# Kernel tuning notes

Hardware: AMD Instinct MI355X
Metric: run time of the kernel (lower is better)

Reference implementation:

```python
import jax, jax.numpy as jnp
import numpy as np

H = 16  # num attention heads
D = 1024  # hidden size
F = 4096  # intermediate size
LN_EPS = 1e-5


def _glorot(key, shape):
    fan_in, fan_out = shape[0], shape[1]
    lim = np.sqrt(6.0 / (fan_in + fan_out))
    return jax.random.uniform(key, shape, jnp.float32, -lim, lim)


def setup_inputs() -> dict:
    key = jax.random.key(0)
    ks = jax.random.split(key, 16)
    inp = {
        'input_tensor': jax.random.normal(ks[0], (4, 1024, D), jnp.float32),
        'ctx_tensor': jax.random.normal(ks[1], (4, 2048, D), jnp.float32),
        'ctx_attn_mask': jnp.zeros((4, 1, 1, 2048), jnp.float32),
        # cross-attention QKV
        'cq_w': _glorot(ks[2], (D, D)), 'cq_b': jnp.zeros((D,)),
        'ck_w': _glorot(ks[3], (D, D)), 'ck_b': jnp.zeros((D,)),
        'cv_w': _glorot(ks[4], (D, D)), 'cv_b': jnp.zeros((D,)),
        # cross output (dense + LN)
        'co_w': _glorot(ks[5], (D, D)), 'co_b': jnp.zeros((D,)),
        'co_g': jnp.ones((D,)), 'co_be': jnp.zeros((D,)),
        # self-attention QKV
        'sq_w': _glorot(ks[6], (D, D)), 'sq_b': jnp.zeros((D,)),
        'sk_w': _glorot(ks[7], (D, D)), 'sk_b': jnp.zeros((D,)),
        'sv_w': _glorot(ks[8], (D, D)), 'sv_b': jnp.zeros((D,)),
        # self-attention output
        'so_w': _glorot(ks[9], (D, D)), 'so_b': jnp.zeros((D,)),
        'so_g': jnp.ones((D,)), 'so_be': jnp.zeros((D,)),
        # FFN intermediate + output
        'fi_w': _glorot(ks[10], (D, F)), 'fi_b': jnp.zeros((F,)),
        'fo_w': _glorot(ks[11], (F, D)), 'fo_b': jnp.zeros((D,)),
        'fo_g': jnp.ones((D,)), 'fo_be': jnp.zeros((D,)),
    }
    return inp


def _split_heads(x):
    b, l, _ = x.shape
    return x.reshape(b, l, H, D // H)


def _mha(x, ctx, mask, qw, qb, kw, kb, vw, vb):
    # manual QK^T/sqrt(d) -> +mask -> softmax -> V (dropout=0 / eval)
    q = _split_heads(x @ qw + qb)       # [b, lq, h, d]
    k = _split_heads(ctx @ kw + kb)     # [b, lk, h, d]
    v = _split_heads(ctx @ vw + vb)
    scores = jnp.einsum('bqhd,bkhd->bhqk', q, k) / np.sqrt(D // H).astype(np.float32)
    if mask is not None:
        scores = scores + mask
    probs = jax.nn.softmax(scores, axis=-1)
    out = jnp.einsum('bhqk,bkhd->bqhd', probs, v)
    return out.reshape(x.shape[0], x.shape[1], D)


def _self_output(h, residual, w, b, g, be):
    h = h @ w + b
    h = h + residual
    mu = jnp.mean(h, axis=-1, keepdims=True)
    var = jnp.mean(jnp.square(h - mu), axis=-1, keepdims=True)
    return (h - mu) * jax.lax.rsqrt(var + LN_EPS) * g + be


def reference(input_tensor, ctx_tensor, ctx_attn_mask,
              cq_w, cq_b, ck_w, ck_b, cv_w, cv_b, co_w, co_b, co_g, co_be,
              sq_w, sq_b, sk_w, sk_b, sv_w, sv_b, so_w, so_b, so_g, so_be,
              fi_w, fi_b, fo_w, fo_b, fo_g, fo_be):
    # CrossLayer.forward
    ca = _mha(input_tensor, ctx_tensor, ctx_attn_mask, cq_w, cq_b, ck_w, ck_b, cv_w, cv_b)
    x = _self_output(ca, input_tensor, co_w, co_b, co_g, co_be)
    sa = _mha(x, x, None, sq_w, sq_b, sk_w, sk_b, sv_w, sv_b)
    x = _self_output(sa, x, so_w, so_b, so_g, so_be)
    inter = jax.nn.gelu(x @ fi_w + fi_b, approximate=False)
    x = _self_output(inter, x, fo_w, fo_b, fo_g, fo_be)
    return x
```

## Files before the change

kernel.cpp:

```cpp
#include <hip/hip_runtime.h>
#include <math.h>

typedef unsigned short ushort_t;
typedef __bf16 bf16x8 __attribute__((ext_vector_type(8)));
typedef float f32x4 __attribute__((ext_vector_type(4)));

__device__ __forceinline__ float bf2f(unsigned int u) {
    union { unsigned int i; float f; } v; v.i = u << 16; return v.f;
}
__device__ __forceinline__ ushort_t f2bf(float f) {
    union { float f; unsigned int i; } v; v.f = f;
    unsigned int u = v.i;
    unsigned int r = u + 0x7fffu + ((u >> 16) & 1u);
    return (ushort_t)(r >> 16);
}
__device__ __forceinline__ ushort_t f2bf_hw(float f) {
    union { __bf16 h; ushort_t u; } v; v.h = (__bf16)f; return v.u;
}

template <int N>
__device__ __forceinline__ float ror16f(float x) {
    union { float f; int i; } u; u.f = x;
    u.i = __builtin_amdgcn_mov_dpp(u.i, 0x120 + N, 0xF, 0xF, true);
    return u.f;
}

__device__ __forceinline__ void gload16(const ushort_t* g, ushort_t* l) {
    __builtin_amdgcn_global_load_lds(
        (__attribute__((address_space(1))) void*)g,
        (__attribute__((address_space(3))) void*)l, 16, 0, 0);
}

__global__ void __launch_bounds__(256) cvt_bf16_kernel(
    const float* __restrict__ in, ushort_t* __restrict__ out, int n8)
{
    int i = blockIdx.x * 256 + threadIdx.x;
    if (i >= n8) return;
    size_t off = (size_t)i * 8;
    float4 a = *(const float4*)(in + off);
    float4 b = *(const float4*)(in + off + 4);
    ushort_t o[8] = {f2bf(a.x), f2bf(a.y), f2bf(a.z), f2bf(a.w),
                     f2bf(b.x), f2bf(b.y), f2bf(b.z), f2bf(b.w)};
    *(uint4*)(out + off) = *(const uint4*)o;
}

__global__ void __launch_bounds__(256) wconv_kernel(
    const float* __restrict__ W, ushort_t* __restrict__ Wt, int K, int N)
{
    __shared__ float tile[32][33];
    const int t = threadIdx.x;
    const int k0 = blockIdx.x * 32, n0 = blockIdx.y * 32;
    const int r = t >> 3, c4 = (t & 7) * 4;
    float4 d = *(const float4*)(&W[(size_t)(k0 + r) * N + n0 + c4]);
    tile[r][c4 + 0] = d.x; tile[r][c4 + 1] = d.y;
    tile[r][c4 + 2] = d.z; tile[r][c4 + 3] = d.w;
    __syncthreads();
    ushort_t o[4] = { f2bf(tile[c4 + 0][r]), f2bf(tile[c4 + 1][r]),
                      f2bf(tile[c4 + 2][r]), f2bf(tile[c4 + 3][r]) };
    *(uint2*)(&Wt[(size_t)(n0 + r) * K + k0 + c4]) = *(const uint2*)o;
}

template <int MODE, int BMT, int BNT, int BKT>
__global__ void __launch_bounds__(256) gemm_bt_kernel(
    const ushort_t* __restrict__ A,
    const ushort_t* __restrict__ B0, const ushort_t* __restrict__ B1,
    const ushort_t* __restrict__ B2,
    const float* __restrict__ bias0, const float* __restrict__ bias1,
    const float* __restrict__ bias2,
    ushort_t* __restrict__ C0, ushort_t* __restrict__ C1,
    ushort_t* __restrict__ C2,
    int M, int N, int K)
{
    __shared__ __align__(16) ushort_t As[2][BMT * BKT];
    __shared__ __align__(16) ushort_t Bs[2][BNT * BKT];

    constexpr int WM = BMT / 2;
    constexpr int MIF = WM / 16;
    constexpr int WN = BNT / 2;
    constexpr int NJF = WN / 16;
    constexpr int KK = BKT / 32;
    constexpr int CPR = BKT / 8;
    constexpr int PA = BMT * BKT / 2048;
    constexpr int PB = BNT * BKT / 2048;
    constexpr int LPT = PA + PB;

    const int z = blockIdx.z;
    const ushort_t* Bt = (z == 0) ? B0 : ((z == 1) ? B1 : B2);
    const float* bias = (z == 0) ? bias0 : ((z == 1) ? bias1 : bias2);
    ushort_t* Cout = (z == 0) ? C0 : ((z == 1) ? C1 : C2);

    const int tid = threadIdx.x;
    const int m0 = blockIdx.y * BMT, n0 = blockIdx.x * BNT;
    const int wave = tid >> 6, lane = tid & 63;
    const int wm = wave >> 1, wn = wave & 1;
    const int lr = lane & 15;
    const int lk = (lane >> 4) * 8;

    const ushort_t* Ab = A + (size_t)m0 * K;
    const ushort_t* Bb = Bt + (size_t)n0 * K;

    f32x4 acc[MIF][NJF];
#pragma unroll
    for (int i = 0; i < MIF; i++)
#pragma unroll
        for (int j = 0; j < NJF; j++) acc[i][j] = (f32x4){0.f, 0.f, 0.f, 0.f};

    const int nt = K / BKT;

    auto stage = [&](int buf, int t) {
#pragma unroll
        for (int p = 0; p < PA; p++) {
            int v = p * 256 + tid;
            int row = v / CPR, c = v % CPR;
            gload16(Ab + (size_t)row * K + (size_t)t * BKT + c * 8,
                    &As[buf][v * 8]);
        }
#pragma unroll
        for (int p = 0; p < PB; p++) {
            int v = p * 256 + tid;
            int row = v / CPR, c = v % CPR;
            gload16(Bb + (size_t)row * K + (size_t)t * BKT + c * 8,
                    &Bs[buf][v * 8]);
        }
    };

    stage(0, 0);

    for (int t = 0; t < nt; ++t) {
        const int p = t & 1;
        if (t + 1 < nt) {
            stage(p ^ 1, t + 1);
            asm volatile("s_waitcnt vmcnt(%0)" :: "n"(LPT) : "memory");
        } else {
            asm volatile("s_waitcnt vmcnt(0)" ::: "memory");
        }
        __builtin_amdgcn_s_barrier();

        bf16x8 af[MIF][KK], bfr[NJF][KK];
#pragma unroll
        for (int i = 0; i < MIF; i++)
#pragma unroll
            for (int kk = 0; kk < KK; kk++)
                af[i][kk] = *(const bf16x8*)(&As[p][(wm * WM + i * 16 + lr) * BKT + kk * 32 + lk]);
#pragma unroll
        for (int j = 0; j < NJF; j++)
#pragma unroll
            for (int kk = 0; kk < KK; kk++)
                bfr[j][kk] = *(const bf16x8*)(&Bs[p][(wn * WN + j * 16 + lr) * BKT + kk * 32 + lk]);
#pragma unroll
        for (int kk = 0; kk < KK; kk++)
#pragma unroll
            for (int i = 0; i < MIF; i++)
#pragma unroll
                for (int j = 0; j < NJF; j++)
                    acc[i][j] = __builtin_amdgcn_mfma_f32_16x16x32_bf16(af[i][kk], bfr[j][kk], acc[i][j], 0, 0, 0);

        asm volatile("" ::: "memory");
        __builtin_amdgcn_s_barrier();
    }

    const int rq = (lane >> 4) * 4;
#pragma unroll
    for (int j = 0; j < NJF; j++) {
        const int col = n0 + wn * WN + j * 16 + lr;
        const float bv = bias[col];
#pragma unroll
        for (int i = 0; i < MIF; i++) {
#pragma unroll
            for (int r = 0; r < 4; r++) {
                const int row = m0 + wm * WM + i * 16 + rq + r;
                float v = acc[i][j][r] + bv;
                if (MODE == 2) {
                    v = 0.5f * v * (1.0f + erff(v * 0.70710678118654752f));
                }
                Cout[(size_t)row * N + col] = f2bf(v);
            }
        }
    }
}

__global__ void __launch_bounds__(256) mfma_attn_kernel(
    const ushort_t* __restrict__ Q, const ushort_t* __restrict__ Kt,
    const ushort_t* __restrict__ Vt, const float* __restrict__ mask,
    ushort_t* __restrict__ O, int Lq, int Lk, float scale)
{
    __shared__ __align__(16) ushort_t qs[64][72];
    __shared__ __align__(16) ushort_t ks[64][72];
    __shared__ __align__(16) ushort_t vsT[64][72];
    __shared__ __align__(16) ushort_t ps[4][16][72];

    const int tid = threadIdx.x;
    const int wave = tid >> 6, lane = tid & 63;
    const int quad = lane >> 4, lc = lane & 15;

    const int id = blockIdx.x + (int)gridDim.x * blockIdx.y;
    const int bh = (id & 7) * 8 + ((id >> 3) >> 4);
    const int qt = (id >> 3) & 15;
    const int b = bh >> 4, h = bh & 15;
    const int q0 = qt * 64;
    const size_t qbase = ((size_t)b * Lq) * 1024 + h * 64;
    const size_t kbase = ((size_t)b * Lk) * 1024 + h * 64;
    const float* maskb = mask ? (mask + (size_t)b * Lk) : nullptr;

#pragma unroll
    for (int r = 0; r < 2; r++) {
        int v = r * 256 + tid;
        int row = v >> 3, c8 = (v & 7) * 8;
        *(uint4*)(&qs[row][c8]) = *(const uint4*)(&Q[qbase + (size_t)(q0 + row) * 1024 + c8]);
    }
    __syncthreads();

    bf16x8 qa0 = *(const bf16x8*)(&qs[wave * 16 + lc][quad * 8]);
    bf16x8 qa1 = *(const bf16x8*)(&qs[wave * 16 + lc][32 + quad * 8]);

    f32x4 o[4];
#pragma unroll
    for (int d = 0; d < 4; d++) o[d] = (f32x4){0.f, 0.f, 0.f, 0.f};
    float m_i[4], l_i[4];
#pragma unroll
    for (int r = 0; r < 4; r++) { m_i[r] = -1e30f; l_i[r] = 0.f; }

    const int sr = tid >> 2;
    const int d0c = (tid & 3) * 16;
    const int vswz = (tid & 3) << 3;
    const int vcol = sr ^ vswz;

    const int nt = Lk >> 6;
    size_t gk = kbase + (size_t)sr * 1024 + d0c;

    uint4 kA = *(const uint4*)(Kt + gk);
    uint4 kB = *(const uint4*)(Kt + gk + 8);
    uint4 vA = *(const uint4*)(Vt + gk);
    uint4 vB = *(const uint4*)(Vt + gk + 8);

    for (int t = 0; t < nt; ++t) {
        const int kt = t << 6;
        __syncthreads();
        *(uint4*)(&ks[sr][d0c])     = kA;
        *(uint4*)(&ks[sr][d0c + 8]) = kB;
        {
            const ushort_t* vp = (const ushort_t*)&vA;
            const ushort_t* wp = (const ushort_t*)&vB;
#pragma unroll
            for (int i = 0; i < 8; i++) vsT[d0c + i][vcol]     = vp[i];
#pragma unroll
            for (int i = 0; i < 8; i++) vsT[d0c + 8 + i][vcol] = wp[i];
        }
        if (t + 1 < nt) {
            gk += 64 * 1024;
            kA = *(const uint4*)(Kt + gk);
            kB = *(const uint4*)(Kt + gk + 8);
            vA = *(const uint4*)(Vt + gk);
            vB = *(const uint4*)(Vt + gk + 8);
        }
        __syncthreads();

        float mk[4];
#pragma unroll
        for (int g = 0; g < 4; g++)
            mk[g] = maskb ? maskb[kt + g * 16 + lc] : 0.f;

        f32x4 s[4];
        __builtin_amdgcn_s_setprio(1);
#pragma unroll
        for (int g = 0; g < 4; g++) {
            bf16x8 k0 = *(const bf16x8*)(&ks[g * 16 + lc][quad * 8]);
            bf16x8 k1 = *(const bf16x8*)(&ks[g * 16 + lc][32 + quad * 8]);
            f32x4 zz = (f32x4){0.f, 0.f, 0.f, 0.f};
            zz = __builtin_amdgcn_mfma_f32_16x16x32_bf16(qa0, k0, zz, 0, 0, 0);
            zz = __builtin_amdgcn_mfma_f32_16x16x32_bf16(qa1, k1, zz, 0, 0, 0);
            s[g] = zz;
        }
        __builtin_amdgcn_s_setprio(0);

        float alpha[4];
#pragma unroll
        for (int r = 0; r < 4; r++) {
            float v0 = s[0][r] * scale + mk[0];
            float v1 = s[1][r] * scale + mk[1];
            float v2 = s[2][r] * scale + mk[2];
            float v3 = s[3][r] * scale + mk[3];
            float mx = fmaxf(fmaxf(v0, v1), fmaxf(v2, v3));
            mx = fmaxf(mx, ror16f<1>(mx));
            mx = fmaxf(mx, ror16f<2>(mx));
            mx = fmaxf(mx, ror16f<4>(mx));
            mx = fmaxf(mx, ror16f<8>(mx));
            float mnew = fmaxf(m_i[r], mx);
            alpha[r] = __expf(m_i[r] - mnew);
            m_i[r] = mnew;
            float p0 = __expf(v0 - mnew);
            float p1 = __expf(v1 - mnew);
            float p2 = __expf(v2 - mnew);
            float p3 = __expf(v3 - mnew);
            ps[wave][quad * 4 + r][lc]      = f2bf_hw(p0);
            ps[wave][quad * 4 + r][16 + lc] = f2bf_hw(p1);
            ps[wave][quad * 4 + r][32 + lc] = f2bf_hw(p2);
            ps[wave][quad * 4 + r][48 + lc] = f2bf_hw(p3);
            float psum = (p0 + p1) + (p2 + p3);
            psum += ror16f<1>(psum);
            psum += ror16f<2>(psum);
            psum += ror16f<4>(psum);
            psum += ror16f<8>(psum);
            l_i[r] = l_i[r] * alpha[r] + psum;
        }
#pragma unroll
        for (int d = 0; d < 4; d++)
#pragma unroll
            for (int r = 0; r < 4; r++) o[d][r] *= alpha[r];

        __builtin_amdgcn_s_setprio(1);
#pragma unroll
        for (int kk = 0; kk < 2; kk++) {
            bf16x8 pa = *(const bf16x8*)(&ps[wave][lc][kk * 32 + quad * 8]);
#pragma unroll
            for (int d = 0; d < 4; d++) {
                int dr = d * 16 + lc;
                bf16x8 vb = *(const bf16x8*)(&vsT[dr][(kk * 32 + quad * 8) ^ (d << 3)]);
                o[d] = __builtin_amdgcn_mfma_f32_16x16x32_bf16(pa, vb, o[d], 0, 0, 0);
            }
        }
        __builtin_amdgcn_s_setprio(0);
    }

#pragma unroll
    for (int d = 0; d < 4; d++) {
#pragma unroll
        for (int r = 0; r < 4; r++) {
            float val = o[d][r] / l_i[r];
            O[qbase + (size_t)(q0 + wave * 16 + quad * 4 + r) * 1024 + d * 16 + lc] = f2bf_hw(val);
        }
    }
}

template <bool RES_F32, bool OUT_F32>
__global__ void __launch_bounds__(256) ln_kernel(
    const ushort_t* __restrict__ Hbuf, const void* __restrict__ Res,
    const float* __restrict__ gamma, const float* __restrict__ beta,
    void* __restrict__ Out)
{
    const int row = blockIdx.x;
    const int tid = threadIdx.x;
    const size_t base = (size_t)row * 1024 + tid * 4;

    uint2 hh = *(const uint2*)(Hbuf + base);
    float v[4];
    v[0] = bf2f(hh.x & 0xffffu);
    v[1] = bf2f(hh.x >> 16);
    v[2] = bf2f(hh.y & 0xffffu);
    v[3] = bf2f(hh.y >> 16);
    if (RES_F32) {
        float4 rv = *(const float4*)((const float*)Res + base);
        v[0] += rv.x; v[1] += rv.y; v[2] += rv.z; v[3] += rv.w;
    } else {
        uint2 rr = *(const uint2*)((const ushort_t*)Res + base);
        v[0] += bf2f(rr.x & 0xffffu);
        v[1] += bf2f(rr.x >> 16);
        v[2] += bf2f(rr.y & 0xffffu);
        v[3] += bf2f(rr.y >> 16);
    }

    float s = v[0] + v[1] + v[2] + v[3];
    float s2 = v[0]*v[0] + v[1]*v[1] + v[2]*v[2] + v[3]*v[3];
#pragma unroll
    for (int o = 1; o < 64; o <<= 1) {
        s += __shfl_xor(s, o, 64);
        s2 += __shfl_xor(s2, o, 64);
    }
    __shared__ float red[8];
    const int wv = tid >> 6, ln_ = tid & 63;
    if (ln_ == 0) { red[wv] = s; red[wv + 4] = s2; }
    __syncthreads();
    s = red[0] + red[1] + red[2] + red[3];
    s2 = red[4] + red[5] + red[6] + red[7];
    const float mu = s * (1.0f / 1024.0f);
    const float var = s2 * (1.0f / 1024.0f) - mu * mu;
    const float rstd = rsqrtf(var + 1e-5f);

    float4 gv = *(const float4*)(&gamma[tid * 4]);
    float4 bv = *(const float4*)(&beta[tid * 4]);
    float o0 = (v[0] - mu) * rstd * gv.x + bv.x;
    float o1 = (v[1] - mu) * rstd * gv.y + bv.y;
    float o2 = (v[2] - mu) * rstd * gv.z + bv.z;
    float o3 = (v[3] - mu) * rstd * gv.w + bv.w;

    if (OUT_F32) {
        float4 of = {o0, o1, o2, o3};
        *(float4*)((float*)Out + base) = of;
    } else {
        ushort_t ob[4] = {f2bf(o0), f2bf(o1), f2bf(o2), f2bf(o3)};
        *(uint2*)((ushort_t*)Out + base) = *(uint2*)ob;
    }
}

extern "C" void kernel_launch(void* const* d_in, const int* in_sizes, int n_in,
                              void* d_out, int out_size, void* d_ws, size_t ws_size,
                              hipStream_t stream)
{
    const float* input = (const float*)d_in[0];
    const float* ctx   = (const float*)d_in[1];
    const float* mask  = (const float*)d_in[2];
    const float* cq_w = (const float*)d_in[3],  *cq_b = (const float*)d_in[4];
    const float* ck_w = (const float*)d_in[5],  *ck_b = (const float*)d_in[6];
    const float* cv_w = (const float*)d_in[7],  *cv_b = (const float*)d_in[8];
    const float* co_w = (const float*)d_in[9],  *co_b = (const float*)d_in[10];
    const float* co_g = (const float*)d_in[11], *co_be = (const float*)d_in[12];
    const float* sq_w = (const float*)d_in[13], *sq_b = (const float*)d_in[14];
    const float* sk_w = (const float*)d_in[15], *sk_b = (const float*)d_in[16];
    const float* sv_w = (const float*)d_in[17], *sv_b = (const float*)d_in[18];
    const float* so_w = (const float*)d_in[19], *so_b = (const float*)d_in[20];
    const float* so_g = (const float*)d_in[21], *so_be = (const float*)d_in[22];
    const float* fi_w = (const float*)d_in[23], *fi_b = (const float*)d_in[24];
    const float* fo_w = (const float*)d_in[25], *fo_b = (const float*)d_in[26];
    const float* fo_g = (const float*)d_in[27], *fo_be = (const float*)d_in[28];

    char* p = (char*)d_ws;
    const size_t MB = 1024 * 1024;
    ushort_t* Bq   = (ushort_t*)(p + 0 * MB);
    ushort_t* Bk   = (ushort_t*)(p + 8 * MB);
    ushort_t* Bv   = (ushort_t*)(p + 24 * MB);
    ushort_t* Ba   = (ushort_t*)(p + 40 * MB);
    ushort_t* Bh   = (ushort_t*)(p + 48 * MB);
    ushort_t* Bx1  = (ushort_t*)(p + 56 * MB);
    ushort_t* Bx2  = (ushort_t*)(p + 64 * MB);
    ushort_t* Bi   = Bk;
    ushort_t* Xctx = Ba;
    ushort_t* Xin  = Bx2;
    ushort_t* WtA  = (ushort_t*)(p + 56 * MB);
    ushort_t* WtB  = (ushort_t*)(p + 58 * MB);
    ushort_t* WtC  = (ushort_t*)(p + 60 * MB);
    ushort_t* WtD  = (ushort_t*)(p + 64 * MB);
    ushort_t* WtE  = (ushort_t*)(p + 66 * MB);
    ushort_t* WtF  = (ushort_t*)(p + 68 * MB);
    ushort_t* WtG  = (ushort_t*)(p + 0 * MB);

    const float scale = 0.125f;
    dim3 blk(256);

    cvt_bf16_kernel<<<2048, blk, 0, stream>>>(input, Xin, 524288);
    cvt_bf16_kernel<<<4096, blk, 0, stream>>>(ctx, Xctx, 1048576);

    wconv_kernel<<<dim3(32, 32), blk, 0, stream>>>(cq_w, WtA, 1024, 1024);
    wconv_kernel<<<dim3(32, 32), blk, 0, stream>>>(ck_w, WtB, 1024, 1024);
    wconv_kernel<<<dim3(32, 32), blk, 0, stream>>>(cv_w, WtC, 1024, 1024);
    gemm_bt_kernel<0, 64, 64, 64><<<dim3(16, 64, 1), blk, 0, stream>>>(
        Xin, WtA, WtA, WtA, cq_b, cq_b, cq_b, Bq, Bq, Bq, 4096, 1024, 1024);
    gemm_bt_kernel<0, 64, 64, 64><<<dim3(16, 128, 2), blk, 0, stream>>>(
        Xctx, WtB, WtC, WtC, ck_b, cv_b, cv_b, Bk, Bv, Bv, 8192, 1024, 1024);
    mfma_attn_kernel<<<dim3(16, 64), blk, 0, stream>>>(Bq, Bk, Bv, mask, Ba, 1024, 2048, scale);
    wconv_kernel<<<dim3(32, 32), blk, 0, stream>>>(co_w, WtA, 1024, 1024);
    gemm_bt_kernel<0, 64, 64, 64><<<dim3(16, 64, 1), blk, 0, stream>>>(
        Ba, WtA, WtA, WtA, co_b, co_b, co_b, Bh, Bh, Bh, 4096, 1024, 1024);
    ln_kernel<true, false><<<dim3(4096), blk, 0, stream>>>(Bh, input, co_g, co_be, Bx1);

    wconv_kernel<<<dim3(32, 32), blk, 0, stream>>>(sq_w, WtD, 1024, 1024);
    wconv_kernel<<<dim3(32, 32), blk, 0, stream>>>(sk_w, WtE, 1024, 1024);
    wconv_kernel<<<dim3(32, 32), blk, 0, stream>>>(sv_w, WtF, 1024, 1024);
    gemm_bt_kernel<0, 64, 64, 64><<<dim3(16, 64, 3), blk, 0, stream>>>(
        Bx1, WtD, WtE, WtF, sq_b, sk_b, sv_b, Bq, Bk, Bv, 4096, 1024, 1024);
    mfma_attn_kernel<<<dim3(16, 64), blk, 0, stream>>>(Bq, Bk, Bv, nullptr, Ba, 1024, 1024, scale);
    wconv_kernel<<<dim3(32, 32), blk, 0, stream>>>(so_w, WtD, 1024, 1024);
    gemm_bt_kernel<0, 64, 64, 64><<<dim3(16, 64, 1), blk, 0, stream>>>(
        Ba, WtD, WtD, WtD, so_b, so_b, so_b, Bh, Bh, Bh, 4096, 1024, 1024);
    ln_kernel<false, false><<<dim3(4096), blk, 0, stream>>>(Bh, Bx1, so_g, so_be, Bx2);

    wconv_kernel<<<dim3(32, 128), blk, 0, stream>>>(fi_w, WtG, 1024, 4096);
    gemm_bt_kernel<2, 128, 128, 32><<<dim3(32, 32, 1), blk, 0, stream>>>(
        Bx2, WtG, WtG, WtG, fi_b, fi_b, fi_b, Bi, Bi, Bi, 4096, 4096, 1024);
    wconv_kernel<<<dim3(128, 32), blk, 0, stream>>>(fo_w, WtG, 4096, 1024);
    gemm_bt_kernel<0, 64, 64, 64><<<dim3(16, 64, 1), blk, 0, stream>>>(
        Bi, WtG, WtG, WtG, fo_b, fo_b, fo_b, Bh, Bh, Bh, 4096, 1024, 4096);
    ln_kernel<false, true><<<dim3(4096), blk, 0, stream>>>(Bh, Bx2, fo_g, fo_be, (float*)d_out);
}
```

Baseline: 699.3 us.

## Merge cross-attention QKV GEMMs, enlarge GEMM M-tile, add lazy softmax rescale

The GEMM kernel now takes two A inputs with per-z row counts, so the cross-attention Q projection (4096 rows) and the K/V projections (8192 rows) run as one launch, with blocks past a slice's rows exiting early. The 1024-wide GEMMs move from 64x64 to 128x64 tiles to get more reuse per block. In flash attention, the running max and the rescale of the output accumulator are skipped when the new block max exceeds the old one by no more than 8 across the wave. This removes exp and multiply work, at the cost of fewer GEMM blocks for occupancy and a looser bound on exponent growth.

```diff
diff --git a/kernel.cpp b/kernel.cpp
--- a/kernel.cpp
+++ b/kernel.cpp
@@ -62,14 +62,15 @@
 
 template <int MODE, int BMT, int BNT, int BKT>
 __global__ void __launch_bounds__(256) gemm_bt_kernel(
-    const ushort_t* __restrict__ A,
+    const ushort_t* __restrict__ A0, const ushort_t* __restrict__ A1,
+    int M0, int M1,
     const ushort_t* __restrict__ B0, const ushort_t* __restrict__ B1,
     const ushort_t* __restrict__ B2,
     const float* __restrict__ bias0, const float* __restrict__ bias1,
     const float* __restrict__ bias2,
     ushort_t* __restrict__ C0, ushort_t* __restrict__ C1,
     ushort_t* __restrict__ C2,
-    int M, int N, int K)
+    int N, int K)
 {
     __shared__ __align__(16) ushort_t As[2][BMT * BKT];
     __shared__ __align__(16) ushort_t Bs[2][BNT * BKT];
@@ -85,12 +86,15 @@
     constexpr int LPT = PA + PB;
 
     const int z = blockIdx.z;
+    const ushort_t* A = (z == 0) ? A0 : A1;
+    const int Mz = (z == 0) ? M0 : M1;
     const ushort_t* Bt = (z == 0) ? B0 : ((z == 1) ? B1 : B2);
     const float* bias = (z == 0) ? bias0 : ((z == 1) ? bias1 : bias2);
     ushort_t* Cout = (z == 0) ? C0 : ((z == 1) ? C1 : C2);
 
     const int tid = threadIdx.x;
     const int m0 = blockIdx.y * BMT, n0 = blockIdx.x * BNT;
+    if (m0 >= Mz) return;
     const int wave = tid >> 6, lane = tid & 63;
     const int wm = wave >> 1, wn = wave & 1;
     const int lr = lane & 15;
@@ -274,6 +278,7 @@
         __builtin_amdgcn_s_setprio(0);
 
         float alpha[4];
+        bool need = false;
 #pragma unroll
         for (int r = 0; r < 4; r++) {
             float v0 = s[0][r] * scale + mk[0];
@@ -285,9 +290,16 @@
             mx = fmaxf(mx, ror16f<2>(mx));
             mx = fmaxf(mx, ror16f<4>(mx));
             mx = fmaxf(mx, ror16f<8>(mx));
-            float mnew = fmaxf(m_i[r], mx);
-            alpha[r] = __expf(m_i[r] - mnew);
-            m_i[r] = mnew;
+            float mnew;
+            if (__all(mx - m_i[r] <= 8.0f)) {
+                alpha[r] = 1.0f;
+                mnew = m_i[r];
+            } else {
+                mnew = fmaxf(m_i[r], mx);
+                alpha[r] = __expf(m_i[r] - mnew);
+                m_i[r] = mnew;
+                need = true;
+            }
             float p0 = __expf(v0 - mnew);
             float p1 = __expf(v1 - mnew);
             float p2 = __expf(v2 - mnew);
@@ -303,10 +315,12 @@
             psum += ror16f<8>(psum);
             l_i[r] = l_i[r] * alpha[r] + psum;
         }
-#pragma unroll
-        for (int d = 0; d < 4; d++)
-#pragma unroll
-            for (int r = 0; r < 4; r++) o[d][r] *= alpha[r];
+        if (need) {
+#pragma unroll
+            for (int d = 0; d < 4; d++)
+#pragma unroll
+                for (int r = 0; r < 4; r++) o[d][r] *= alpha[r];
+        }
 
         __builtin_amdgcn_s_setprio(1);
 #pragma unroll
@@ -442,32 +456,36 @@
     wconv_kernel<<<dim3(32, 32), blk, 0, stream>>>(cq_w, WtA, 1024, 1024);
     wconv_kernel<<<dim3(32, 32), blk, 0, stream>>>(ck_w, WtB, 1024, 1024);
     wconv_kernel<<<dim3(32, 32), blk, 0, stream>>>(cv_w, WtC, 1024, 1024);
-    gemm_bt_kernel<0, 64, 64, 64><<<dim3(16, 64, 1), blk, 0, stream>>>(
-        Xin, WtA, WtA, WtA, cq_b, cq_b, cq_b, Bq, Bq, Bq, 4096, 1024, 1024);
-    gemm_bt_kernel<0, 64, 64, 64><<<dim3(16, 128, 2), blk, 0, stream>>>(
-        Xctx, WtB, WtC, WtC, ck_b, cv_b, cv_b, Bk, Bv, Bv, 8192, 1024, 1024);
+    gemm_bt_kernel<0, 128, 64, 64><<<dim3(16, 64, 3), blk, 0, stream>>>(
+        Xin, Xctx, 4096, 8192, WtA, WtB, WtC, cq_b, ck_b, cv_b,
+        Bq, Bk, Bv, 1024, 1024);
     mfma_attn_kernel<<<dim3(16, 64), blk, 0, stream>>>(Bq, Bk, Bv, mask, Ba, 1024, 2048, scale);
     wconv_kernel<<<dim3(32, 32), blk, 0, stream>>>(co_w, WtA, 1024, 1024);
-    gemm_bt_kernel<0, 64, 64, 64><<<dim3(16, 64, 1), blk, 0, stream>>>(
-        Ba, WtA, WtA, WtA, co_b, co_b, co_b, Bh, Bh, Bh, 4096, 1024, 1024);
+    gemm_bt_kernel<0, 128, 64, 64><<<dim3(16, 32, 1), blk, 0, stream>>>(
+        Ba, Ba, 4096, 4096, WtA, WtA, WtA, co_b, co_b, co_b,
+        Bh, Bh, Bh, 1024, 1024);
     ln_kernel<true, false><<<dim3(4096), blk, 0, stream>>>(Bh, input, co_g, co_be, Bx1);
 
     wconv_kernel<<<dim3(32, 32), blk, 0, stream>>>(sq_w, WtD, 1024, 1024);
     wconv_kernel<<<dim3(32, 32), blk, 0, stream>>>(sk_w, WtE, 1024, 1024);
     wconv_kernel<<<dim3(32, 32), blk, 0, stream>>>(sv_w, WtF, 1024, 1024);
-    gemm_bt_kernel<0, 64, 64, 64><<<dim3(16, 64, 3), blk, 0, stream>>>(
-        Bx1, WtD, WtE, WtF, sq_b, sk_b, sv_b, Bq, Bk, Bv, 4096, 1024, 1024);
+    gemm_bt_kernel<0, 128, 64, 64><<<dim3(16, 32, 3), blk, 0, stream>>>(
+        Bx1, Bx1, 4096, 4096, WtD, WtE, WtF, sq_b, sk_b, sv_b,
+        Bq, Bk, Bv, 1024, 1024);
     mfma_attn_kernel<<<dim3(16, 64), blk, 0, stream>>>(Bq, Bk, Bv, nullptr, Ba, 1024, 1024, scale);
     wconv_kernel<<<dim3(32, 32), blk, 0, stream>>>(so_w, WtD, 1024, 1024);
-    gemm_bt_kernel<0, 64, 64, 64><<<dim3(16, 64, 1), blk, 0, stream>>>(
-        Ba, WtD, WtD, WtD, so_b, so_b, so_b, Bh, Bh, Bh, 4096, 1024, 1024);
+    gemm_bt_kernel<0, 128, 64, 64><<<dim3(16, 32, 1), blk, 0, stream>>>(
+        Ba, Ba, 4096, 4096, WtD, WtD, WtD, so_b, so_b, so_b,
+        Bh, Bh, Bh, 1024, 1024);
     ln_kernel<false, false><<<dim3(4096), blk, 0, stream>>>(Bh, Bx1, so_g, so_be, Bx2);
 
     wconv_kernel<<<dim3(32, 128), blk, 0, stream>>>(fi_w, WtG, 1024, 4096);
     gemm_bt_kernel<2, 128, 128, 32><<<dim3(32, 32, 1), blk, 0, stream>>>(
-        Bx2, WtG, WtG, WtG, fi_b, fi_b, fi_b, Bi, Bi, Bi, 4096, 4096, 1024);
+        Bx2, Bx2, 4096, 4096, WtG, WtG, WtG, fi_b, fi_b, fi_b,
+        Bi, Bi, Bi, 4096, 1024);
     wconv_kernel<<<dim3(128, 32), blk, 0, stream>>>(fo_w, WtG, 4096, 1024);
-    gemm_bt_kernel<0, 64, 64, 64><<<dim3(16, 64, 1), blk, 0, stream>>>(
-        Bi, WtG, WtG, WtG, fo_b, fo_b, fo_b, Bh, Bh, Bh, 4096, 1024, 4096);
+    gemm_bt_kernel<0, 128, 64, 64><<<dim3(16, 32, 1), blk, 0, stream>>>(
+        Bi, Bi, 4096, 4096, WtG, WtG, WtG, fo_b, fo_b, fo_b,
+        Bh, Bh, Bh, 1024, 4096);
     ln_kernel<false, true><<<dim3(4096), blk, 0, stream>>>(Bh, Bx2, fo_g, fo_be, (float*)d_out);
 }
```

Measured after the change: 665.7 us. 4.8% less time.
